# Kernel tuning notes

Measured on AMD Instinct MI355X. Metric: run time of the kernel, lower is better.

## Reference

```python
import jax, jax.numpy as jnp
import numpy as np
from jax import lax

B, D, K = 65536, 256, 32  # batch, num_latent_dims, flow_depth


def setup_inputs() -> dict:
    key = jax.random.key(0)
    k1, k2, k3, k4, k5 = jax.random.split(key, 5)
    X = jax.random.normal(k1, (B, D), dtype=jnp.float32)
    h = jax.random.normal(k2, (B, D), dtype=jnp.float32)  # passed through, unused by planar math
    u = jax.random.normal(k3, (K, D), dtype=jnp.float32) * 0.1
    w = jax.random.normal(k4, (K, D), dtype=jnp.float32) * 0.1
    b = jax.random.normal(k5, (K,), dtype=jnp.float32) * 0.1
    return {"X": X, "h": h, "u": u, "w": w, "b": b}


def _planar_chain(z0, u, w, b):
    """Sequential planar normalizing flow: z_{k+1} = z_k + u_hat_k * tanh(w_k.z_k + b_k)."""

    def step(z, params):
        u_k, w_k, b_k = params  # (D,), (D,), scalar
        # enforce invertibility: u_hat so that w.u_hat >= -1
        wu = jnp.dot(w_k, u_k)
        u_hat = u_k + (jax.nn.softplus(wu) - 1.0 - wu) * w_k / jnp.dot(w_k, w_k)
        lin = z @ w_k + b_k              # (B,)
        t = jnp.tanh(lin)                # (B,)
        z_new = z + t[:, None] * u_hat[None, :]
        # psi = (1 - t^2) w ; log|det J| = log|1 + psi.u_hat|
        log_det = jnp.log(jnp.abs(1.0 + (1.0 - t * t) * jnp.dot(w_k, u_hat)) + 1e-8)
        return z_new, log_det

    z_final, log_dets = lax.scan(step, z0, (u, w, b))
    return z_final, log_dets  # (B, D), (K, B)


def reference(X, h, u, w, b):
    z = X.reshape(X.shape[0], X.shape[1])  # view(B, D, -1) then view(B, D) -> (B, D)
    z_final, log_det_jacobians = _planar_chain(z, u, w, b)
    return z_final, log_det_jacobians
```

## Files before the change

### kernel.cpp

```cpp
#include <hip/hip_runtime.h>


#define B_ 65536
#define D_ 256
#define K_ 32
#define ROWS 256
#define XT_STRIDE 264
#define UT_STRIDE 260

__global__ __launch_bounds__(256) void nf_fused(const float* __restrict__ X,
                                                const float* __restrict__ u_in,
                                                const float* __restrict__ w_in,
                                                const float* __restrict__ b_in,
                                                float* __restrict__ out) {
  __shared__ float wT1[8192];
  __shared__ float uT2[32 * UT_STRIDE];
  __shared__ float XtP[8448];
  __shared__ float Gm[32 * 33];
  __shared__ float cs_s[32], coefs_s[32], bfs_s[32];

  const int t = threadIdx.x;
  const int lane = t & 63;
  const int wv = t >> 6;
  const int rg = lane >> 2;
  const int kq = lane & 3;
  const int row0 = blockIdx.x * ROWS;
  const int rp = t & 127;
  const int ch = t >> 7;
  const int xoff = wv * 64 + rg * 4;
  const int kw = t >> 3;
  const int d0g = (t & 7) * 32;

  {
    float4 tmp[8];
    const float4* wp = (const float4*)(w_in + kw * 256 + d0g);
#pragma unroll
    for (int j = 0; j < 8; ++j) tmp[j] = wp[j];
#pragma unroll
    for (int j = 0; j < 8; ++j) {
      wT1[(d0g + j * 4 + 0) * 32 + kw] = tmp[j].x;
      wT1[(d0g + j * 4 + 1) * 32 + kw] = tmp[j].y;
      wT1[(d0g + j * 4 + 2) * 32 + kw] = tmp[j].z;
      wT1[(d0g + j * 4 + 3) * 32 + kw] = tmp[j].w;
    }
    const float4* up = (const float4*)(u_in + kw * 256 + d0g);
#pragma unroll
    for (int j = 0; j < 8; ++j) tmp[j] = up[j];
    float4* ud = (float4*)&uT2[kw * UT_STRIDE + d0g];
#pragma unroll
    for (int j = 0; j < 8; ++j) ud[j] = tmp[j];
    if (t < 32) bfs_s[t] = b_in[t];
  }

  float4 pf[8];
  const float* xbase = X + (size_t)(row0 + 2 * rp) * 256 + ch * 16;
  auto load_stage = [&](int s) {
    const float4* a = (const float4*)(xbase + s * 32);
    const float4* b = (const float4*)(xbase + 256 + s * 32);
#pragma unroll
    for (int j = 0; j < 4; ++j) pf[j] = a[j];
#pragma unroll
    for (int j = 0; j < 4; ++j) pf[4 + j] = b[j];
  };
  auto store_stage = [&]() {
#pragma unroll
    for (int cc = 0; cc < 16; ++cc) {
      const float* fa = (const float*)&pf[cc >> 2];
      const float* fb = (const float*)&pf[4 + (cc >> 2)];
      *(float2*)&XtP[(ch * 16 + cc) * XT_STRIDE + 2 * rp] =
          make_float2(fa[cc & 3], fb[cc & 3]);
    }
  };
  load_stage(0);
  __syncthreads();

  {
    int qd = t >> 6, which = (t >> 5) & 1, j = t & 31;
    int dlo = qd * 64;
    float acc = 0.f;
    if (which == 0) {
#pragma unroll 8
      for (int d = 0; d < 64; ++d)
        acc = fmaf(wT1[(dlo + d) * 32 + j], uT2[j * UT_STRIDE + dlo + d], acc);
    } else {
#pragma unroll 8
      for (int d = 0; d < 64; ++d) {
        float wvv = wT1[(dlo + d) * 32 + j];
        acc = fmaf(wvv, wvv, acc);
      }
    }
    XtP[t] = acc;
  }
  __syncthreads();
  if (t < 32) {
    float wu = XtP[t] + XtP[64 + t] + XtP[128 + t] + XtP[192 + t];
    float ww = XtP[32 + t] + XtP[96 + t] + XtP[160 + t] + XtP[224 + t];
    float sp = fmaxf(wu, 0.f) + log1pf(__expf(-fabsf(wu)));
    coefs_s[t] = (sp - 1.f - wu) / ww;
    cs_s[t] = sp - 1.f;
  }
  __syncthreads();

  {
    float ck = coefs_s[kw];
    float4* ud = (float4*)&uT2[kw * UT_STRIDE + d0g];
#pragma unroll
    for (int j = 0; j < 8; ++j) {
      float4 uvv = ud[j];
      uvv.x = fmaf(ck, wT1[(d0g + j * 4 + 0) * 32 + kw], uvv.x);
      uvv.y = fmaf(ck, wT1[(d0g + j * 4 + 1) * 32 + kw], uvv.y);
      uvv.z = fmaf(ck, wT1[(d0g + j * 4 + 2) * 32 + kw], uvv.z);
      uvv.w = fmaf(ck, wT1[(d0g + j * 4 + 3) * 32 + kw], uvv.w);
      ud[j] = uvv;
    }
  }
  __syncthreads();

  {
    int j = t & 31, kg = t >> 5;
    float g0 = 0.f, g1 = 0.f, g2 = 0.f, g3 = 0.f;
#pragma unroll 4
    for (int d = 0; d < 256; ++d) {
      float uj = uT2[j * UT_STRIDE + d];
      g0 = fmaf(uj, wT1[d * 32 + kg], g0);
      g1 = fmaf(uj, wT1[d * 32 + kg + 8], g1);
      g2 = fmaf(uj, wT1[d * 32 + kg + 16], g2);
      g3 = fmaf(uj, wT1[d * 32 + kg + 24], g3);
    }
    Gm[kg * 33 + j] = g0;
    Gm[(kg + 8) * 33 + j] = g1;
    Gm[(kg + 16) * 33 + j] = g2;
    Gm[(kg + 24) * 33 + j] = g3;
  }

  float p[4][8];
#pragma unroll
  for (int a = 0; a < 4; ++a)
#pragma unroll
    for (int b2 = 0; b2 < 8; ++b2) p[a][b2] = 0.f;

  for (int s = 0; s < 8; ++s) {
    store_stage();
    __syncthreads();
    if (s < 7) load_stage(s + 1);
#pragma unroll 8
    for (int d = 0; d < 32; ++d) {
      float4 xv = *(const float4*)&XtP[d * XT_STRIDE + xoff];
      const float* wrow = &wT1[(s * 32 + d) * 32 + kq * 8];
      float4 w0 = *(const float4*)wrow;
      float4 w1 = *(const float4*)(wrow + 4);
      const float xr[4] = {xv.x, xv.y, xv.z, xv.w};
      const float wk[8] = {w0.x, w0.y, w0.z, w0.w, w1.x, w1.y, w1.z, w1.w};
#pragma unroll
      for (int a = 0; a < 4; ++a)
#pragma unroll
        for (int b2 = 0; b2 < 8; ++b2) p[a][b2] = fmaf(xr[a], wk[b2], p[a][b2]);
    }
    __syncthreads();
  }

#pragma unroll
  for (int a = 0; a < 4; ++a) {
    float4* dst = (float4*)&XtP[(xoff + a) * 32 + kq * 8];
    dst[0] = make_float4(p[a][0], p[a][1], p[a][2], p[a][3]);
    dst[1] = make_float4(p[a][4], p[a][5], p[a][6], p[a][7]);
  }
  __syncthreads();
  load_stage(0);

  {
    float pfull[32];
    const float4* ps = (const float4*)&XtP[t * 32];
#pragma unroll
    for (int j = 0; j < 8; ++j) {
      float4 v = ps[j];
      pfull[j * 4 + 0] = v.x + bfs_s[j * 4 + 0];
      pfull[j * 4 + 1] = v.y + bfs_s[j * 4 + 1];
      pfull[j * 4 + 2] = v.z + bfs_s[j * 4 + 2];
      pfull[j * 4 + 3] = v.w + bfs_s[j * 4 + 3];
    }
    float tvv[32];
#pragma unroll
    for (int k = 0; k < 32; ++k) {
      float la = pfull[k], lb = 0.f;
      const float* gp = &Gm[k * 33];
#pragma unroll
      for (int j = 0; j + 1 < k; j += 2) {
        la = fmaf(tvv[j], gp[j], la);
        lb = fmaf(tvv[j + 1], gp[j + 1], lb);
      }
      if (k & 1) la = fmaf(tvv[k - 1], gp[k - 1], la);
      float lin = la + lb;
      float e = __expf(2.f * lin);
      float tk = 1.f - 2.f / (e + 1.f);
      tvv[k] = tk;
      wT1[k * 256 + t] = tk;
      float val = fabsf(fmaf(1.f - tk * tk, cs_s[k], 1.f)) + 1e-8f;
      out[(size_t)B_ * D_ + (size_t)k * B_ + row0 + t] = __logf(val);
    }
  }
  __syncthreads();

  for (int s = 0; s < 8; ++s) {
    store_stage();
    __syncthreads();
    if (s < 7) load_stage(s + 1);
    float acc[4][8];
#pragma unroll
    for (int dd = 0; dd < 8; ++dd) {
      float4 xv = *(const float4*)&XtP[(kq * 8 + dd) * XT_STRIDE + xoff];
      acc[0][dd] = xv.x;
      acc[1][dd] = xv.y;
      acc[2][dd] = xv.z;
      acc[3][dd] = xv.w;
    }
#pragma unroll 8
    for (int k = 0; k < 32; ++k) {
      float4 t4 = *(const float4*)&wT1[k * 256 + xoff];
      const float* ur = &uT2[k * UT_STRIDE + s * 32 + kq * 8];
      float4 u0 = *(const float4*)ur;
      float4 u1 = *(const float4*)(ur + 4);
      const float tr[4] = {t4.x, t4.y, t4.z, t4.w};
      const float uk[8] = {u0.x, u0.y, u0.z, u0.w, u1.x, u1.y, u1.z, u1.w};
#pragma unroll
      for (int a = 0; a < 4; ++a)
#pragma unroll
        for (int b2 = 0; b2 < 8; ++b2) acc[a][b2] = fmaf(tr[a], uk[b2], acc[a][b2]);
    }
#pragma unroll
    for (int a = 0; a < 4; ++a) {
      float4* op = (float4*)(out + (size_t)(row0 + xoff + a) * 256 + s * 32 + kq * 8);
      op[0] = make_float4(acc[a][0], acc[a][1], acc[a][2], acc[a][3]);
      op[1] = make_float4(acc[a][4], acc[a][5], acc[a][6], acc[a][7]);
    }
    __syncthreads();
  }
}

extern "C" void kernel_launch(void* const* d_in, const int* in_sizes, int n_in,
                              void* d_out, int out_size, void* d_ws, size_t ws_size,
                              hipStream_t stream) {
  const float* X = (const float*)d_in[0];
  const float* u = (const float*)d_in[2];
  const float* w = (const float*)d_in[3];
  const float* b = (const float*)d_in[4];
  float* out = (float*)d_out;

  nf_fused<<<B_ / ROWS, 256, 0, stream>>>(X, u, w, b, out);
}
```

Before: 211.1 us.

## Restructure kernel to 128-row blocks with direct global X reads and algebraic Gram setup

Rewrites the fused planar-flow kernel to process 128 rows per 512-thread block. X is read straight from global memory per row instead of being staged and transposed through shared memory, and X is re-read from global for the output pass. The Gram matrices are computed directly from global u/w and the u_hat correction is folded in algebraically (G = U·W + coef·W·W), which removes several setup phases. Shared memory drops and occupancy goes up, at the cost of uncoalesced row-strided global loads, a second read of X, and a serial tanh recurrence that now runs on only 128 of the 512 threads.

Measured after the change: 279.0 us. 32.2% more time.

```diff
diff --git a/kernel.cpp b/kernel.cpp
--- a/kernel.cpp
+++ b/kernel.cpp
@@ -4,97 +4,74 @@
 #define B_ 65536
 #define D_ 256
 #define K_ 32
-#define ROWS 256
-#define XT_STRIDE 264
-#define UT_STRIDE 260
-
-__global__ __launch_bounds__(256) void nf_fused(const float* __restrict__ X,
-                                                const float* __restrict__ u_in,
-                                                const float* __restrict__ w_in,
-                                                const float* __restrict__ b_in,
-                                                float* __restrict__ out) {
-  __shared__ float wT1[8192];
-  __shared__ float uT2[32 * UT_STRIDE];
-  __shared__ float XtP[8448];
+#define ROWS 128
+#define NTHR 512
+#define WT_STRIDE 36
+#define US_STRIDE 260
+#define P_OFF 4096
+
+__global__ __launch_bounds__(NTHR, 4) void nf_fused(const float* __restrict__ X,
+                                                    const float* __restrict__ u_in,
+                                                    const float* __restrict__ w_in,
+                                                    const float* __restrict__ b_in,
+                                                    float* __restrict__ out) {
+  __shared__ float wT[256 * WT_STRIDE];
+  __shared__ float us[32 * US_STRIDE];
   __shared__ float Gm[32 * 33];
+  __shared__ float Gm2[32 * 33];
   __shared__ float cs_s[32], coefs_s[32], bfs_s[32];
 
   const int t = threadIdx.x;
-  const int lane = t & 63;
-  const int wv = t >> 6;
-  const int rg = lane >> 2;
-  const int kq = lane & 3;
   const int row0 = blockIdx.x * ROWS;
-  const int rp = t & 127;
-  const int ch = t >> 7;
-  const int xoff = wv * 64 + rg * 4;
-  const int kw = t >> 3;
-  const int d0g = (t & 7) * 32;
-
-  {
-    float4 tmp[8];
-    const float4* wp = (const float4*)(w_in + kw * 256 + d0g);
-#pragma unroll
-    for (int j = 0; j < 8; ++j) tmp[j] = wp[j];
-#pragma unroll
-    for (int j = 0; j < 8; ++j) {
-      wT1[(d0g + j * 4 + 0) * 32 + kw] = tmp[j].x;
-      wT1[(d0g + j * 4 + 1) * 32 + kw] = tmp[j].y;
-      wT1[(d0g + j * 4 + 2) * 32 + kw] = tmp[j].z;
-      wT1[(d0g + j * 4 + 3) * 32 + kw] = tmp[j].w;
-    }
-    const float4* up = (const float4*)(u_in + kw * 256 + d0g);
-#pragma unroll
-    for (int j = 0; j < 8; ++j) tmp[j] = up[j];
-    float4* ud = (float4*)&uT2[kw * UT_STRIDE + d0g];
-#pragma unroll
-    for (int j = 0; j < 8; ++j) ud[j] = tmp[j];
+  const int r = t & 127;
+  const int ko = t >> 7;
+
+  {
+    const int k = t & 31;
+    const int d0 = (t >> 5) * 16;
+    float4 wv4[4];
+    const float4* wp = (const float4*)(w_in + k * 256 + d0);
+#pragma unroll
+    for (int q = 0; q < 4; ++q) wv4[q] = wp[q];
+#pragma unroll
+    for (int q = 0; q < 4; ++q) {
+      const float* f = (const float*)&wv4[q];
+#pragma unroll
+      for (int i = 0; i < 4; ++i) wT[(d0 + q * 4 + i) * WT_STRIDE + k] = f[i];
+    }
     if (t < 32) bfs_s[t] = b_in[t];
   }
 
-  float4 pf[8];
-  const float* xbase = X + (size_t)(row0 + 2 * rp) * 256 + ch * 16;
-  auto load_stage = [&](int s) {
-    const float4* a = (const float4*)(xbase + s * 32);
-    const float4* b = (const float4*)(xbase + 256 + s * 32);
-#pragma unroll
-    for (int j = 0; j < 4; ++j) pf[j] = a[j];
-#pragma unroll
-    for (int j = 0; j < 4; ++j) pf[4 + j] = b[j];
-  };
-  auto store_stage = [&]() {
-#pragma unroll
-    for (int cc = 0; cc < 16; ++cc) {
-      const float* fa = (const float*)&pf[cc >> 2];
-      const float* fb = (const float*)&pf[4 + (cc >> 2)];
-      *(float2*)&XtP[(ch * 16 + cc) * XT_STRIDE + 2 * rp] =
-          make_float2(fa[cc & 3], fb[cc & 3]);
-    }
-  };
-  load_stage(0);
-  __syncthreads();
-
-  {
-    int qd = t >> 6, which = (t >> 5) & 1, j = t & 31;
-    int dlo = qd * 64;
-    float acc = 0.f;
-    if (which == 0) {
-#pragma unroll 8
-      for (int d = 0; d < 64; ++d)
-        acc = fmaf(wT1[(dlo + d) * 32 + j], uT2[j * UT_STRIDE + dlo + d], acc);
-    } else {
-#pragma unroll 8
-      for (int d = 0; d < 64; ++d) {
-        float wvv = wT1[(dlo + d) * 32 + j];
-        acc = fmaf(wvv, wvv, acc);
-      }
-    }
-    XtP[t] = acc;
-  }
-  __syncthreads();
+  {
+    const int j = t & 31;
+    const int kg = t >> 5;
+    const float4* uj = (const float4*)(u_in + j * 256);
+    const float4* wj = (const float4*)(w_in + j * 256);
+    const float4* wk0 = (const float4*)(w_in + kg * 256);
+    const float4* wk1 = (const float4*)(w_in + (kg + 16) * 256);
+    float m10 = 0.f, m11 = 0.f, m20 = 0.f, m21 = 0.f;
+#pragma unroll 4
+    for (int q = 0; q < 64; ++q) {
+      float4 a = uj[q], bw = wj[q], c0 = wk0[q], c1 = wk1[q];
+      m10 = fmaf(a.x, c0.x, m10); m10 = fmaf(a.y, c0.y, m10);
+      m10 = fmaf(a.z, c0.z, m10); m10 = fmaf(a.w, c0.w, m10);
+      m11 = fmaf(a.x, c1.x, m11); m11 = fmaf(a.y, c1.y, m11);
+      m11 = fmaf(a.z, c1.z, m11); m11 = fmaf(a.w, c1.w, m11);
+      m20 = fmaf(bw.x, c0.x, m20); m20 = fmaf(bw.y, c0.y, m20);
+      m20 = fmaf(bw.z, c0.z, m20); m20 = fmaf(bw.w, c0.w, m20);
+      m21 = fmaf(bw.x, c1.x, m21); m21 = fmaf(bw.y, c1.y, m21);
+      m21 = fmaf(bw.z, c1.z, m21); m21 = fmaf(bw.w, c1.w, m21);
+    }
+    Gm[kg * 33 + j] = m10;
+    Gm[(kg + 16) * 33 + j] = m11;
+    Gm2[kg * 33 + j] = m20;
+    Gm2[(kg + 16) * 33 + j] = m21;
+  }
+  __syncthreads();
+
   if (t < 32) {
-    float wu = XtP[t] + XtP[64 + t] + XtP[128 + t] + XtP[192 + t];
-    float ww = XtP[32 + t] + XtP[96 + t] + XtP[160 + t] + XtP[224 + t];
+    float wu = Gm[t * 33 + t];
+    float ww = Gm2[t * 33 + t];
     float sp = fmaxf(wu, 0.f) + log1pf(__expf(-fabsf(wu)));
     coefs_s[t] = (sp - 1.f - wu) / ww;
     cs_s[t] = sp - 1.f;
@@ -102,83 +79,71 @@
   __syncthreads();
 
   {
-    float ck = coefs_s[kw];
-    float4* ud = (float4*)&uT2[kw * UT_STRIDE + d0g];
-#pragma unroll
-    for (int j = 0; j < 8; ++j) {
-      float4 uvv = ud[j];
-      uvv.x = fmaf(ck, wT1[(d0g + j * 4 + 0) * 32 + kw], uvv.x);
-      uvv.y = fmaf(ck, wT1[(d0g + j * 4 + 1) * 32 + kw], uvv.y);
-      uvv.z = fmaf(ck, wT1[(d0g + j * 4 + 2) * 32 + kw], uvv.z);
-      uvv.w = fmaf(ck, wT1[(d0g + j * 4 + 3) * 32 + kw], uvv.w);
-      ud[j] = uvv;
-    }
-  }
-  __syncthreads();
-
-  {
-    int j = t & 31, kg = t >> 5;
-    float g0 = 0.f, g1 = 0.f, g2 = 0.f, g3 = 0.f;
-#pragma unroll 4
-    for (int d = 0; d < 256; ++d) {
-      float uj = uT2[j * UT_STRIDE + d];
-      g0 = fmaf(uj, wT1[d * 32 + kg], g0);
-      g1 = fmaf(uj, wT1[d * 32 + kg + 8], g1);
-      g2 = fmaf(uj, wT1[d * 32 + kg + 16], g2);
-      g3 = fmaf(uj, wT1[d * 32 + kg + 24], g3);
-    }
-    Gm[kg * 33 + j] = g0;
-    Gm[(kg + 8) * 33 + j] = g1;
-    Gm[(kg + 16) * 33 + j] = g2;
-    Gm[(kg + 24) * 33 + j] = g3;
-  }
-
-  float p[4][8];
-#pragma unroll
-  for (int a = 0; a < 4; ++a)
-#pragma unroll
-    for (int b2 = 0; b2 < 8; ++b2) p[a][b2] = 0.f;
-
-  for (int s = 0; s < 8; ++s) {
-    store_stage();
-    __syncthreads();
-    if (s < 7) load_stage(s + 1);
-#pragma unroll 8
-    for (int d = 0; d < 32; ++d) {
-      float4 xv = *(const float4*)&XtP[d * XT_STRIDE + xoff];
-      const float* wrow = &wT1[(s * 32 + d) * 32 + kq * 8];
-      float4 w0 = *(const float4*)wrow;
-      float4 w1 = *(const float4*)(wrow + 4);
-      const float xr[4] = {xv.x, xv.y, xv.z, xv.w};
-      const float wk[8] = {w0.x, w0.y, w0.z, w0.w, w1.x, w1.y, w1.z, w1.w};
-#pragma unroll
-      for (int a = 0; a < 4; ++a)
-#pragma unroll
-        for (int b2 = 0; b2 < 8; ++b2) p[a][b2] = fmaf(xr[a], wk[b2], p[a][b2]);
-    }
-    __syncthreads();
-  }
-
-#pragma unroll
-  for (int a = 0; a < 4; ++a) {
-    float4* dst = (float4*)&XtP[(xoff + a) * 32 + kq * 8];
-    dst[0] = make_float4(p[a][0], p[a][1], p[a][2], p[a][3]);
-    dst[1] = make_float4(p[a][4], p[a][5], p[a][6], p[a][7]);
-  }
-  __syncthreads();
-  load_stage(0);
-
-  {
+    {
+      const int k0 = t >> 5, j0 = t & 31;
+      Gm[k0 * 33 + j0] = fmaf(coefs_s[j0], Gm2[k0 * 33 + j0], Gm[k0 * 33 + j0]);
+      const int k1 = k0 + 16;
+      Gm[k1 * 33 + j0] = fmaf(coefs_s[j0], Gm2[k1 * 33 + j0], Gm[k1 * 33 + j0]);
+    }
+    const int k = t >> 4;
+    const int d0 = (t & 15) * 16;
+    const float ck = coefs_s[k];
+    const float4* up = (const float4*)(u_in + k * 256 + d0);
+    const float4* wp = (const float4*)(w_in + k * 256 + d0);
+    float4* ud = (float4*)&us[k * US_STRIDE + d0];
+#pragma unroll
+    for (int q = 0; q < 4; ++q) {
+      float4 uv = up[q], wv = wp[q];
+      uv.x = fmaf(ck, wv.x, uv.x);
+      uv.y = fmaf(ck, wv.y, uv.y);
+      uv.z = fmaf(ck, wv.z, uv.z);
+      uv.w = fmaf(ck, wv.w, uv.w);
+      ud[q] = uv;
+    }
+  }
+  __syncthreads();
+
+  float p[8];
+#pragma unroll
+  for (int b2 = 0; b2 < 8; ++b2) p[b2] = 0.f;
+  {
+    const int kb = ko * 8;
+    const float4* xrow = (const float4*)(X + (size_t)(row0 + r) * 256);
+#pragma unroll 2
+    for (int c = 0; c < 16; ++c) {
+      float4 xq[4];
+#pragma unroll
+      for (int q = 0; q < 4; ++q) xq[q] = xrow[c * 4 + q];
+#pragma unroll
+      for (int i = 0; i < 16; ++i) {
+        const int d = c * 16 + i;
+        float4 w0 = *(const float4*)&wT[d * WT_STRIDE + kb];
+        float4 w1 = *(const float4*)&wT[d * WT_STRIDE + kb + 4];
+        const float xd = ((const float*)xq)[i];
+        p[0] = fmaf(xd, w0.x, p[0]);
+        p[1] = fmaf(xd, w0.y, p[1]);
+        p[2] = fmaf(xd, w0.z, p[2]);
+        p[3] = fmaf(xd, w0.w, p[3]);
+        p[4] = fmaf(xd, w1.x, p[4]);
+        p[5] = fmaf(xd, w1.y, p[5]);
+        p[6] = fmaf(xd, w1.z, p[6]);
+        p[7] = fmaf(xd, w1.w, p[7]);
+      }
+    }
+  }
+  __syncthreads();
+
+  {
+    const int kb = ko * 8;
+#pragma unroll
+    for (int b2 = 0; b2 < 8; ++b2) wT[P_OFF + (kb + b2) * 128 + r] = p[b2];
+  }
+  __syncthreads();
+
+  if (t < 128) {
     float pfull[32];
-    const float4* ps = (const float4*)&XtP[t * 32];
-#pragma unroll
-    for (int j = 0; j < 8; ++j) {
-      float4 v = ps[j];
-      pfull[j * 4 + 0] = v.x + bfs_s[j * 4 + 0];
-      pfull[j * 4 + 1] = v.y + bfs_s[j * 4 + 1];
-      pfull[j * 4 + 2] = v.z + bfs_s[j * 4 + 2];
-      pfull[j * 4 + 3] = v.w + bfs_s[j * 4 + 3];
-    }
+#pragma unroll
+    for (int j = 0; j < 32; ++j) pfull[j] = wT[P_OFF + j * 128 + t] + bfs_s[j];
     float tvv[32];
 #pragma unroll
     for (int k = 0; k < 32; ++k) {
@@ -194,46 +159,44 @@
       float e = __expf(2.f * lin);
       float tk = 1.f - 2.f / (e + 1.f);
       tvv[k] = tk;
-      wT1[k * 256 + t] = tk;
+      wT[k * 128 + t] = tk;
       float val = fabsf(fmaf(1.f - tk * tk, cs_s[k], 1.f)) + 1e-8f;
       out[(size_t)B_ * D_ + (size_t)k * B_ + row0 + t] = __logf(val);
     }
   }
   __syncthreads();
 
-  for (int s = 0; s < 8; ++s) {
-    store_stage();
-    __syncthreads();
-    if (s < 7) load_stage(s + 1);
-    float acc[4][8];
-#pragma unroll
-    for (int dd = 0; dd < 8; ++dd) {
-      float4 xv = *(const float4*)&XtP[(kq * 8 + dd) * XT_STRIDE + xoff];
-      acc[0][dd] = xv.x;
-      acc[1][dd] = xv.y;
-      acc[2][dd] = xv.z;
-      acc[3][dd] = xv.w;
-    }
-#pragma unroll 8
+  for (int pass = 0; pass < 2; ++pass) {
+    const int c0 = ko * 64 + pass * 32;
+    float acc[32];
+    {
+      const float4* xrow = (const float4*)(X + (size_t)(row0 + r) * 256 + c0);
+#pragma unroll
+      for (int q = 0; q < 8; ++q) {
+        float4 v = xrow[q];
+        acc[q * 4 + 0] = v.x;
+        acc[q * 4 + 1] = v.y;
+        acc[q * 4 + 2] = v.z;
+        acc[q * 4 + 3] = v.w;
+      }
+    }
+#pragma unroll 2
     for (int k = 0; k < 32; ++k) {
-      float4 t4 = *(const float4*)&wT1[k * 256 + xoff];
-      const float* ur = &uT2[k * UT_STRIDE + s * 32 + kq * 8];
-      float4 u0 = *(const float4*)ur;
-      float4 u1 = *(const float4*)(ur + 4);
-      const float tr[4] = {t4.x, t4.y, t4.z, t4.w};
-      const float uk[8] = {u0.x, u0.y, u0.z, u0.w, u1.x, u1.y, u1.z, u1.w};
-#pragma unroll
-      for (int a = 0; a < 4; ++a)
-#pragma unroll
-        for (int b2 = 0; b2 < 8; ++b2) acc[a][b2] = fmaf(tr[a], uk[b2], acc[a][b2]);
-    }
-#pragma unroll
-    for (int a = 0; a < 4; ++a) {
-      float4* op = (float4*)(out + (size_t)(row0 + xoff + a) * 256 + s * 32 + kq * 8);
-      op[0] = make_float4(acc[a][0], acc[a][1], acc[a][2], acc[a][3]);
-      op[1] = make_float4(acc[a][4], acc[a][5], acc[a][6], acc[a][7]);
-    }
-    __syncthreads();
+      float tk = wT[k * 128 + r];
+      const float4* uu = (const float4*)&us[k * US_STRIDE + c0];
+#pragma unroll
+      for (int q = 0; q < 8; ++q) {
+        float4 uv = uu[q];
+        acc[q * 4 + 0] = fmaf(tk, uv.x, acc[q * 4 + 0]);
+        acc[q * 4 + 1] = fmaf(tk, uv.y, acc[q * 4 + 1]);
+        acc[q * 4 + 2] = fmaf(tk, uv.z, acc[q * 4 + 2]);
+        acc[q * 4 + 3] = fmaf(tk, uv.w, acc[q * 4 + 3]);
+      }
+    }
+    float4* orow = (float4*)(out + (size_t)(row0 + r) * 256 + c0);
+#pragma unroll
+    for (int q = 0; q < 8; ++q)
+      orow[q] = make_float4(acc[q * 4 + 0], acc[q * 4 + 1], acc[q * 4 + 2], acc[q * 4 + 3]);
   }
 }
 
@@ -246,5 +209,5 @@
   const float* b = (const float*)d_in[4];
   float* out = (float*)d_out;
 
-  nf_fused<<<B_ / ROWS, 256, 0, stream>>>(X, u, w, b, out);
+  nf_fused<<<B_ / ROWS, NTHR, 0, stream>>>(X, u, w, b, out);
 }
```

## Precompute flow parameters in a setup kernel and halve rows per block

Applied to the files above, without the earlier changes.

Moves the per-block computation of u_hat, the Gram matrix G and the softplus coefficients into a separate single-block kernel that writes them to workspace. The main kernel now loads them directly. It also processes 128 rows per block instead of 256, uses a swizzled X transpose tile, and in the second pass reads X straight from global memory instead of restaging it through shared memory. The goals are to drop redundant per-block setup, cut shared memory use to raise occupancy, and remove the second pass's syncs. The costs are an extra launch, a serial recurrence that now runs on only 128 of 256 threads, and a second global read of X.

After: 204.5 us. -3.1%, faster.

```diff
diff --git a/kernel.cpp b/kernel.cpp
--- a/kernel.cpp
+++ b/kernel.cpp
@@ -3,237 +3,241 @@
 
 #define B_ 65536
 #define D_ 256
-#define K_ 32
-#define ROWS 256
-#define XT_STRIDE 264
-#define UT_STRIDE 260
+#define ROWS 128
+#define GRID (B_ / ROWS)
+
+#define WS_WT 0
+#define WS_UH 8192
+#define WS_G  16384
+#define WS_C  17408
+
+#define SW(c) (4 * (((c) + ((c) >> 3)) & 7))
+
+__global__ __launch_bounds__(256) void nf_gen(const float* __restrict__ u_in,
+                                              const float* __restrict__ w_in,
+                                              float* __restrict__ ws) {
+  __shared__ float wTg[8192];
+  __shared__ float ug[8192];
+  __shared__ float wu_s[32], ww_s[32], coefs_s[32];
+  const int t = threadIdx.x;
+  {
+    const int k = t & 31, d0 = (t >> 5) * 32;
+    const float4* wp = (const float4*)(w_in + k * 256 + d0);
+#pragma unroll
+    for (int q = 0; q < 8; ++q) {
+      float4 v = wp[q];
+      wTg[(d0 + q * 4 + 0) * 32 + k] = v.x;
+      wTg[(d0 + q * 4 + 1) * 32 + k] = v.y;
+      wTg[(d0 + q * 4 + 2) * 32 + k] = v.z;
+      wTg[(d0 + q * 4 + 3) * 32 + k] = v.w;
+    }
+#pragma unroll
+    for (int q = 0; q < 8; ++q)
+      ((float4*)ug)[t + 256 * q] = ((const float4*)u_in)[t + 256 * q];
+  }
+  __syncthreads();
+  const int k = t & 31, jg = t >> 5;
+  float m1[4] = {0.f, 0.f, 0.f, 0.f}, m2[4] = {0.f, 0.f, 0.f, 0.f};
+#pragma unroll 4
+  for (int dc = 0; dc < 64; ++dc) {
+    float wk[4];
+    float4 wj[4], uj[4];
+#pragma unroll
+    for (int i = 0; i < 4; ++i) wk[i] = wTg[(dc * 4 + i) * 32 + k];
+#pragma unroll
+    for (int i = 0; i < 4; ++i) wj[i] = *(const float4*)&wTg[(dc * 4 + i) * 32 + jg * 4];
+#pragma unroll
+    for (int i = 0; i < 4; ++i) uj[i] = *(const float4*)&ug[(jg * 4 + i) * 256 + dc * 4];
+#pragma unroll
+    for (int i = 0; i < 4; ++i) {
+      m1[i] = fmaf(uj[i].x, wk[0], m1[i]);
+      m1[i] = fmaf(uj[i].y, wk[1], m1[i]);
+      m1[i] = fmaf(uj[i].z, wk[2], m1[i]);
+      m1[i] = fmaf(uj[i].w, wk[3], m1[i]);
+    }
+    const float* w0 = (const float*)&wj[0];
+    const float* w1 = (const float*)&wj[1];
+    const float* w2 = (const float*)&wj[2];
+    const float* w3 = (const float*)&wj[3];
+#pragma unroll
+    for (int i = 0; i < 4; ++i) {
+      m2[i] = fmaf(w0[i], wk[0], m2[i]);
+      m2[i] = fmaf(w1[i], wk[1], m2[i]);
+      m2[i] = fmaf(w2[i], wk[2], m2[i]);
+      m2[i] = fmaf(w3[i], wk[3], m2[i]);
+    }
+  }
+  if ((k >> 2) == jg) {
+    wu_s[k] = m1[k & 3];
+    ww_s[k] = m2[k & 3];
+  }
+  __syncthreads();
+  if (t < 32) {
+    float wu = wu_s[t], ww = ww_s[t];
+    float sp = fmaxf(wu, 0.f) + log1pf(__expf(-fabsf(wu)));
+    coefs_s[t] = (sp - 1.f - wu) / ww;
+    ws[WS_C + t] = sp - 1.f;
+  }
+  __syncthreads();
+#pragma unroll
+  for (int i = 0; i < 4; ++i)
+    ws[WS_G + k * 32 + jg * 4 + i] = fmaf(coefs_s[jg * 4 + i], m2[i], m1[i]);
+  {
+    const int k2 = t >> 3, d0 = (t & 7) * 32;
+    const float ck = coefs_s[k2];
+    const float4* up = (const float4*)(u_in + k2 * 256 + d0);
+    const float4* wp2 = (const float4*)(w_in + k2 * 256 + d0);
+    float4* od = (float4*)(ws + WS_UH + k2 * 256 + d0);
+#pragma unroll
+    for (int q = 0; q < 8; ++q) {
+      float4 uv = up[q], wv = wp2[q];
+      uv.x = fmaf(ck, wv.x, uv.x);
+      uv.y = fmaf(ck, wv.y, uv.y);
+      uv.z = fmaf(ck, wv.z, uv.z);
+      uv.w = fmaf(ck, wv.w, uv.w);
+      od[q] = uv;
+    }
+  }
+#pragma unroll
+  for (int q = 0; q < 8; ++q)
+    ((float4*)(ws + WS_WT))[t + 256 * q] = ((const float4*)wTg)[t + 256 * q];
+}
 
 __global__ __launch_bounds__(256) void nf_fused(const float* __restrict__ X,
-                                                const float* __restrict__ u_in,
-                                                const float* __restrict__ w_in,
                                                 const float* __restrict__ b_in,
+                                                const float* __restrict__ ws,
                                                 float* __restrict__ out) {
-  __shared__ float wT1[8192];
-  __shared__ float uT2[32 * UT_STRIDE];
-  __shared__ float XtP[8448];
-  __shared__ float Gm[32 * 33];
-  __shared__ float cs_s[32], coefs_s[32], bfs_s[32];
-
+  __shared__ float wT[8192];
+  __shared__ float us[8192];
+  __shared__ float Xs[4096];
   const int t = threadIdx.x;
-  const int lane = t & 63;
-  const int wv = t >> 6;
-  const int rg = lane >> 2;
-  const int kq = lane & 3;
   const int row0 = blockIdx.x * ROWS;
-  const int rp = t & 127;
-  const int ch = t >> 7;
-  const int xoff = wv * 64 + rg * 4;
-  const int kw = t >> 3;
-  const int d0g = (t & 7) * 32;
-
-  {
-    float4 tmp[8];
-    const float4* wp = (const float4*)(w_in + kw * 256 + d0g);
-#pragma unroll
-    for (int j = 0; j < 8; ++j) tmp[j] = wp[j];
-#pragma unroll
-    for (int j = 0; j < 8; ++j) {
-      wT1[(d0g + j * 4 + 0) * 32 + kw] = tmp[j].x;
-      wT1[(d0g + j * 4 + 1) * 32 + kw] = tmp[j].y;
-      wT1[(d0g + j * 4 + 2) * 32 + kw] = tmp[j].z;
-      wT1[(d0g + j * 4 + 3) * 32 + kw] = tmp[j].w;
-    }
-    const float4* up = (const float4*)(u_in + kw * 256 + d0g);
-#pragma unroll
-    for (int j = 0; j < 8; ++j) tmp[j] = up[j];
-    float4* ud = (float4*)&uT2[kw * UT_STRIDE + d0g];
-#pragma unroll
-    for (int j = 0; j < 8; ++j) ud[j] = tmp[j];
-    if (t < 32) bfs_s[t] = b_in[t];
-  }
-
-  float4 pf[8];
-  const float* xbase = X + (size_t)(row0 + 2 * rp) * 256 + ch * 16;
+  const int xoff = (t >> 6) * 32 + ((t >> 3) & 7) * 4;
+  const int kq4 = (t & 7) * 4;
+  const int row_ld = t >> 3;
+  const int cl = t & 7;
+
+#pragma unroll
+  for (int q = 0; q < 8; ++q)
+    ((float4*)wT)[t + 256 * q] = ((const float4*)(ws + WS_WT))[t + 256 * q];
+#pragma unroll
+  for (int q = 0; q < 8; ++q)
+    ((float4*)us)[t + 256 * q] = ((const float4*)(ws + WS_UH))[t + 256 * q];
+
+  float4 pf[4];
   auto load_stage = [&](int s) {
-    const float4* a = (const float4*)(xbase + s * 32);
-    const float4* b = (const float4*)(xbase + 256 + s * 32);
-#pragma unroll
-    for (int j = 0; j < 4; ++j) pf[j] = a[j];
-#pragma unroll
-    for (int j = 0; j < 4; ++j) pf[4 + j] = b[j];
+#pragma unroll
+    for (int p = 0; p < 4; ++p)
+      pf[p] = *(const float4*)(X + (size_t)(row0 + p * 32 + row_ld) * 256 + s * 32 + cl * 4);
   };
   auto store_stage = [&]() {
 #pragma unroll
-    for (int cc = 0; cc < 16; ++cc) {
-      const float* fa = (const float*)&pf[cc >> 2];
-      const float* fb = (const float*)&pf[4 + (cc >> 2)];
-      *(float2*)&XtP[(ch * 16 + cc) * XT_STRIDE + 2 * rp] =
-          make_float2(fa[cc & 3], fb[cc & 3]);
+    for (int p = 0; p < 4; ++p) {
+      const float f[4] = {pf[p].x, pf[p].y, pf[p].z, pf[p].w};
+#pragma unroll
+      for (int i = 0; i < 4; ++i) {
+        const int c = cl * 4 + i;
+        Xs[c * 128 + ((p * 32 + row_ld + SW(c)) & 127)] = f[i];
+      }
     }
   };
+
   load_stage(0);
   __syncthreads();
 
-  {
-    int qd = t >> 6, which = (t >> 5) & 1, j = t & 31;
-    int dlo = qd * 64;
-    float acc = 0.f;
-    if (which == 0) {
-#pragma unroll 8
-      for (int d = 0; d < 64; ++d)
-        acc = fmaf(wT1[(dlo + d) * 32 + j], uT2[j * UT_STRIDE + dlo + d], acc);
-    } else {
-#pragma unroll 8
-      for (int d = 0; d < 64; ++d) {
-        float wvv = wT1[(dlo + d) * 32 + j];
-        acc = fmaf(wvv, wvv, acc);
-      }
-    }
-    XtP[t] = acc;
-  }
-  __syncthreads();
-  if (t < 32) {
-    float wu = XtP[t] + XtP[64 + t] + XtP[128 + t] + XtP[192 + t];
-    float ww = XtP[32 + t] + XtP[96 + t] + XtP[160 + t] + XtP[224 + t];
-    float sp = fmaxf(wu, 0.f) + log1pf(__expf(-fabsf(wu)));
-    coefs_s[t] = (sp - 1.f - wu) / ww;
-    cs_s[t] = sp - 1.f;
-  }
-  __syncthreads();
-
-  {
-    float ck = coefs_s[kw];
-    float4* ud = (float4*)&uT2[kw * UT_STRIDE + d0g];
-#pragma unroll
-    for (int j = 0; j < 8; ++j) {
-      float4 uvv = ud[j];
-      uvv.x = fmaf(ck, wT1[(d0g + j * 4 + 0) * 32 + kw], uvv.x);
-      uvv.y = fmaf(ck, wT1[(d0g + j * 4 + 1) * 32 + kw], uvv.y);
-      uvv.z = fmaf(ck, wT1[(d0g + j * 4 + 2) * 32 + kw], uvv.z);
-      uvv.w = fmaf(ck, wT1[(d0g + j * 4 + 3) * 32 + kw], uvv.w);
-      ud[j] = uvv;
-    }
-  }
-  __syncthreads();
-
-  {
-    int j = t & 31, kg = t >> 5;
-    float g0 = 0.f, g1 = 0.f, g2 = 0.f, g3 = 0.f;
-#pragma unroll 4
-    for (int d = 0; d < 256; ++d) {
-      float uj = uT2[j * UT_STRIDE + d];
-      g0 = fmaf(uj, wT1[d * 32 + kg], g0);
-      g1 = fmaf(uj, wT1[d * 32 + kg + 8], g1);
-      g2 = fmaf(uj, wT1[d * 32 + kg + 16], g2);
-      g3 = fmaf(uj, wT1[d * 32 + kg + 24], g3);
-    }
-    Gm[kg * 33 + j] = g0;
-    Gm[(kg + 8) * 33 + j] = g1;
-    Gm[(kg + 16) * 33 + j] = g2;
-    Gm[(kg + 24) * 33 + j] = g3;
-  }
-
-  float p[4][8];
+  float p[4][4];
 #pragma unroll
   for (int a = 0; a < 4; ++a)
 #pragma unroll
-    for (int b2 = 0; b2 < 8; ++b2) p[a][b2] = 0.f;
+    for (int b = 0; b < 4; ++b) p[a][b] = 0.f;
 
   for (int s = 0; s < 8; ++s) {
     store_stage();
     __syncthreads();
     if (s < 7) load_stage(s + 1);
 #pragma unroll 8
-    for (int d = 0; d < 32; ++d) {
-      float4 xv = *(const float4*)&XtP[d * XT_STRIDE + xoff];
-      const float* wrow = &wT1[(s * 32 + d) * 32 + kq * 8];
-      float4 w0 = *(const float4*)wrow;
-      float4 w1 = *(const float4*)(wrow + 4);
+    for (int dl = 0; dl < 32; ++dl) {
+      float4 xv = *(const float4*)&Xs[dl * 128 + ((xoff + SW(dl)) & 127)];
+      float4 wv = *(const float4*)&wT[(s * 32 + dl) * 32 + kq4];
       const float xr[4] = {xv.x, xv.y, xv.z, xv.w};
-      const float wk[8] = {w0.x, w0.y, w0.z, w0.w, w1.x, w1.y, w1.z, w1.w};
+      const float wk[4] = {wv.x, wv.y, wv.z, wv.w};
 #pragma unroll
       for (int a = 0; a < 4; ++a)
 #pragma unroll
-        for (int b2 = 0; b2 < 8; ++b2) p[a][b2] = fmaf(xr[a], wk[b2], p[a][b2]);
+        for (int b = 0; b < 4; ++b) p[a][b] = fmaf(xr[a], wk[b], p[a][b]);
     }
     __syncthreads();
   }
 
 #pragma unroll
-  for (int a = 0; a < 4; ++a) {
-    float4* dst = (float4*)&XtP[(xoff + a) * 32 + kq * 8];
-    dst[0] = make_float4(p[a][0], p[a][1], p[a][2], p[a][3]);
-    dst[1] = make_float4(p[a][4], p[a][5], p[a][6], p[a][7]);
-  }
-  __syncthreads();
-  load_stage(0);
-
-  {
+  for (int b = 0; b < 4; ++b)
+    *(float4*)&wT[(kq4 + b) * 128 + xoff] = make_float4(p[0][b], p[1][b], p[2][b], p[3][b]);
+#pragma unroll
+  for (int i = 0; i < 4; ++i) {
+    const int e = t * 4 + i;
+    Xs[(e >> 5) * 33 + (e & 31)] = ws[WS_G + e];
+  }
+  if (t < 32) {
+    Xs[1536 + t] = ws[WS_C + t];
+    Xs[1568 + t] = b_in[t];
+  }
+  __syncthreads();
+
+  if (t < 128) {
     float pfull[32];
-    const float4* ps = (const float4*)&XtP[t * 32];
-#pragma unroll
-    for (int j = 0; j < 8; ++j) {
-      float4 v = ps[j];
-      pfull[j * 4 + 0] = v.x + bfs_s[j * 4 + 0];
-      pfull[j * 4 + 1] = v.y + bfs_s[j * 4 + 1];
-      pfull[j * 4 + 2] = v.z + bfs_s[j * 4 + 2];
-      pfull[j * 4 + 3] = v.w + bfs_s[j * 4 + 3];
-    }
+#pragma unroll
+    for (int j = 0; j < 32; ++j) pfull[j] = wT[j * 128 + t] + Xs[1568 + j];
     float tvv[32];
 #pragma unroll
-    for (int k = 0; k < 32; ++k) {
-      float la = pfull[k], lb = 0.f;
-      const float* gp = &Gm[k * 33];
-#pragma unroll
-      for (int j = 0; j + 1 < k; j += 2) {
+    for (int kk = 0; kk < 32; ++kk) {
+      float la = pfull[kk], lb = 0.f;
+      const float* gp = &Xs[kk * 33];
+#pragma unroll
+      for (int j = 0; j + 1 < kk; j += 2) {
         la = fmaf(tvv[j], gp[j], la);
         lb = fmaf(tvv[j + 1], gp[j + 1], lb);
       }
-      if (k & 1) la = fmaf(tvv[k - 1], gp[k - 1], la);
+      if (kk & 1) la = fmaf(tvv[kk - 1], gp[kk - 1], la);
       float lin = la + lb;
       float e = __expf(2.f * lin);
       float tk = 1.f - 2.f / (e + 1.f);
-      tvv[k] = tk;
-      wT1[k * 256 + t] = tk;
-      float val = fabsf(fmaf(1.f - tk * tk, cs_s[k], 1.f)) + 1e-8f;
-      out[(size_t)B_ * D_ + (size_t)k * B_ + row0 + t] = __logf(val);
-    }
-  }
-  __syncthreads();
-
-  for (int s = 0; s < 8; ++s) {
-    store_stage();
-    __syncthreads();
-    if (s < 7) load_stage(s + 1);
+      tvv[kk] = tk;
+      wT[4096 + kk * 128 + t] = tk;
+      float val = fabsf(fmaf(1.f - tk * tk, Xs[1536 + kk], 1.f)) + 1e-8f;
+      out[(size_t)B_ * D_ + (size_t)kk * B_ + row0 + t] = __logf(val);
+    }
+  }
+  __syncthreads();
+
+  const int cq8 = (t & 7) * 8;
+  for (int cb = 0; cb < 4; ++cb) {
+    const int c0 = cb * 64 + cq8;
     float acc[4][8];
 #pragma unroll
-    for (int dd = 0; dd < 8; ++dd) {
-      float4 xv = *(const float4*)&XtP[(kq * 8 + dd) * XT_STRIDE + xoff];
-      acc[0][dd] = xv.x;
-      acc[1][dd] = xv.y;
-      acc[2][dd] = xv.z;
-      acc[3][dd] = xv.w;
+    for (int a = 0; a < 4; ++a) {
+      const float4 x0 = *(const float4*)(X + (size_t)(row0 + xoff + a) * 256 + c0);
+      const float4 x1 = *(const float4*)(X + (size_t)(row0 + xoff + a) * 256 + c0 + 4);
+      acc[a][0] = x0.x; acc[a][1] = x0.y; acc[a][2] = x0.z; acc[a][3] = x0.w;
+      acc[a][4] = x1.x; acc[a][5] = x1.y; acc[a][6] = x1.z; acc[a][7] = x1.w;
     }
 #pragma unroll 8
-    for (int k = 0; k < 32; ++k) {
-      float4 t4 = *(const float4*)&wT1[k * 256 + xoff];
-      const float* ur = &uT2[k * UT_STRIDE + s * 32 + kq * 8];
-      float4 u0 = *(const float4*)ur;
-      float4 u1 = *(const float4*)(ur + 4);
+    for (int kk = 0; kk < 32; ++kk) {
+      float4 t4 = *(const float4*)&wT[4096 + kk * 128 + xoff];
+      float4 u0 = *(const float4*)&us[kk * 256 + c0];
+      float4 u1 = *(const float4*)&us[kk * 256 + c0 + 4];
       const float tr[4] = {t4.x, t4.y, t4.z, t4.w};
       const float uk[8] = {u0.x, u0.y, u0.z, u0.w, u1.x, u1.y, u1.z, u1.w};
 #pragma unroll
       for (int a = 0; a < 4; ++a)
 #pragma unroll
-        for (int b2 = 0; b2 < 8; ++b2) acc[a][b2] = fmaf(tr[a], uk[b2], acc[a][b2]);
+        for (int b = 0; b < 8; ++b) acc[a][b] = fmaf(tr[a], uk[b], acc[a][b]);
     }
 #pragma unroll
     for (int a = 0; a < 4; ++a) {
-      float4* op = (float4*)(out + (size_t)(row0 + xoff + a) * 256 + s * 32 + kq * 8);
+      float4* op = (float4*)(out + (size_t)(row0 + xoff + a) * 256 + c0);
       op[0] = make_float4(acc[a][0], acc[a][1], acc[a][2], acc[a][3]);
       op[1] = make_float4(acc[a][4], acc[a][5], acc[a][6], acc[a][7]);
     }
-    __syncthreads();
   }
 }
 
@@ -245,6 +249,8 @@
   const float* w = (const float*)d_in[3];
   const float* b = (const float*)d_in[4];
   float* out = (float*)d_out;
-
-  nf_fused<<<B_ / ROWS, 256, 0, stream>>>(X, u, w, b, out);
+  float* ws = (float*)d_ws;
+
+  nf_gen<<<1, 256, 0, stream>>>(u, w, ws);
+  nf_fused<<<GRID, 256, 0, stream>>>(X, b, ws, out);
 }
```
